# Kernel tuning notes

Hardware: AMD Instinct MI355X
Metric: run time of the kernel (lower is better)

The kernel has to match this reference:

```python
import jax, jax.numpy as jnp
import numpy as np

EPS = 1e-3  # batch_norm_epsilon


def _lstm_last(xs, W, U, b):
    """Keras-order LSTM (gates i,f,g,o); returns last hidden state [B,H]."""
    B = xs.shape[0]
    H = U.shape[0]

    def step(carry, xt):
        h, c = carry
        z = xt @ W + h @ U + b  # [B, 4H]
        i, f, g, o = jnp.split(z, 4, axis=-1)
        i = jax.nn.sigmoid(i)
        f = jax.nn.sigmoid(f)
        g = jnp.tanh(g)
        o = jax.nn.sigmoid(o)
        c = f * c + i * g
        h = o * jnp.tanh(c)
        return (h, c), None

    init = (jnp.zeros((B, H), xs.dtype), jnp.zeros((B, H), xs.dtype))
    (h, _), _ = jax.lax.scan(step, init, jnp.swapaxes(xs, 0, 1))
    return h


def setup_inputs() -> dict:
    key = jax.random.key(0)
    ks = jax.random.split(key, 10)
    B, T, C, H = 32, 512, 512, 512
    s_in = 1.0 / np.sqrt(C)
    s_rec = 1.0 / np.sqrt(H)
    return {
        "x": jax.random.normal(ks[0], (B, T, C), jnp.float32),
        # BatchNorm params (inference / moving stats)
        "gamma": jnp.ones((C,), jnp.float32),
        "beta": jnp.zeros((C,), jnp.float32),
        "moving_mean": jax.random.normal(ks[1], (C,), jnp.float32) * 0.1,
        "moving_var": jnp.abs(jax.random.normal(ks[2], (C,), jnp.float32)) * 0.1 + 1.0,
        # forward-direction LSTM
        "Wf": jax.random.normal(ks[3], (C, 4 * H), jnp.float32) * s_in,
        "Uf": jax.random.normal(ks[4], (H, 4 * H), jnp.float32) * s_rec,
        "bf": jnp.zeros((4 * H,), jnp.float32),
        # backward-direction LSTM
        "Wb": jax.random.normal(ks[5], (C, 4 * H), jnp.float32) * s_in,
        "Ub": jax.random.normal(ks[6], (H, 4 * H), jnp.float32) * s_rec,
        "bb": jnp.zeros((4 * H,), jnp.float32),
    }


def reference(x, gamma, beta, moving_mean, moving_var, Wf, Uf, bf, Wb, Ub, bb):
    # BatchNorm (inference) over last axis
    inv = jax.lax.rsqrt(moving_var + EPS)
    xn = (x - moving_mean) * inv * gamma + beta
    # Bidirectional LSTM, merge_mode='concat', return_sequences=False
    h_fwd = _lstm_last(xn, Wf, Uf, bf)
    h_bwd = _lstm_last(xn[:, ::-1, :], Wb, Ub, bb)
    return jnp.concatenate([h_fwd, h_bwd], axis=-1)  # [B, 2H]
```

## Files before the change

### kernel.cpp

```cpp
#include <hip/hip_runtime.h>
#include <stdint.h>

typedef __attribute__((ext_vector_type(8))) short short8;
typedef __attribute__((ext_vector_type(4))) float f32x4;
typedef __attribute__((ext_vector_type(2))) float f32x2;
typedef __attribute__((ext_vector_type(4))) unsigned int u32x4;
typedef __attribute__((ext_vector_type(2))) unsigned int u32x2;

#define NB 32
#define NBH 16
#define NT 512
#define NC 512
#define NH 512
#define NG 2048
#define WPG 16
#define NWG 64
#define UPW 32

__device__ __forceinline__ float bf2f(unsigned short u){
  union { unsigned int i; float f; } v; v.i = ((unsigned int)u) << 16; return v.f;
}
__device__ __forceinline__ unsigned short f2bf(float f){
  union { float f; unsigned int i; } v; v.f = f;
  unsigned int r = v.i + 0x7fffu + ((v.i >> 16) & 1u);
  return (unsigned short)(r >> 16);
}
__device__ __forceinline__ bool dt_fp32(const void* gamma){
  return ((const unsigned short*)gamma)[0] != 0x3F80;
}
__device__ __forceinline__ float ldv(const void* p, size_t i, bool f32){
  return f32 ? ((const float*)p)[i] : bf2f(((const unsigned short*)p)[i]);
}
__device__ __forceinline__ short8 frag_from_f32(const float* p){
  short8 r;
  #pragma unroll
  for (int j = 0; j < 8; ++j) r[j] = (short)f2bf(p[j]);
  return r;
}
__device__ __forceinline__ float sigm(float x){ return 1.f/(1.f + __expf(-x)); }
__device__ __forceinline__ float tanh_(float x){ return 1.f - 2.f/(1.f + __expf(2.f*x)); }

__device__ __forceinline__ unsigned int permhi(unsigned int hi, unsigned int lo){
  return __builtin_amdgcn_perm(hi, lo, 0x07060302u);
}

__device__ __forceinline__ unsigned int llc_load_u32(const unsigned int* p){
  unsigned int r;
  asm volatile("global_load_dword %0, %1, off sc0 sc1\n\ts_waitcnt vmcnt(0)"
               : "=v"(r) : "v"(p) : "memory");
  return r;
}
__device__ __forceinline__ void llc_store_u32(unsigned int* p, unsigned int v){
  asm volatile("global_store_dword %0, %1, off sc0 sc1" :: "v"(p), "v"(v) : "memory");
}
__device__ __forceinline__ void tag_load(const unsigned int* p0, u32x4 r[8]){
  asm volatile(
    "global_load_dwordx4 %0, %8, off sc0 sc1\n\t"
    "global_load_dwordx4 %1, %8, off offset:16 sc0 sc1\n\t"
    "global_load_dwordx4 %2, %8, off offset:128 sc0 sc1\n\t"
    "global_load_dwordx4 %3, %8, off offset:144 sc0 sc1\n\t"
    "global_load_dwordx4 %4, %8, off offset:256 sc0 sc1\n\t"
    "global_load_dwordx4 %5, %8, off offset:272 sc0 sc1\n\t"
    "global_load_dwordx4 %6, %8, off offset:384 sc0 sc1\n\t"
    "global_load_dwordx4 %7, %8, off offset:400 sc0 sc1\n\t"
    "s_waitcnt vmcnt(0)"
    : "=&v"(r[0]), "=&v"(r[1]), "=&v"(r[2]), "=&v"(r[3]),
      "=&v"(r[4]), "=&v"(r[5]), "=&v"(r[6]), "=&v"(r[7])
    : "v"(p0) : "memory");
}
__device__ __forceinline__ void tag_store(unsigned int* p, unsigned int lo, unsigned int hi){
  u32x2 v; v[0] = lo; v[1] = hi;
  asm volatile("global_store_dwordx2 %0, %1, off sc0 sc1" :: "v"(p), "v"(v) : "memory");
}

__global__ void k_init(const void* __restrict__ gamma,
                       const void* __restrict__ beta,
                       const void* __restrict__ mmean,
                       const void* __restrict__ mvar,
                       float* __restrict__ scale, float* __restrict__ shift,
                       unsigned int* __restrict__ hbuf, unsigned int* __restrict__ flags){
  bool f32 = dt_fp32(gamma);
  int tid = blockIdx.x * 256 + threadIdx.x;
  if (blockIdx.x == 0){
    for (int c = threadIdx.x; c < NC; c += 256){
      float s = ldv(gamma, c, f32) * rsqrtf(ldv(mvar, c, f32) + 1e-3f);
      scale[c] = s;
      shift[c] = ldv(beta, c, f32) - ldv(mmean, c, f32) * s;
    }
    if (threadIdx.x < 128) flags[threadIdx.x] = 0u;
  }
  for (int i = tid; i < 4*2*NBH*NH; i += gridDim.x * 256) hbuf[i] = 0u;
}

__global__ void k_xcast(const void* __restrict__ x, const void* __restrict__ gamma,
                        unsigned short* __restrict__ x2){
  bool f32 = dt_fp32(gamma);
  int i = blockIdx.x * 256 + threadIdx.x;
  int c8 = i & 63;
  int rest = i >> 6;
  int t = rest & (NT - 1);
  int b = rest >> 9;
  size_t src = ((size_t)b * NT + t) * NC + c8 * 8;
  size_t dst = ((size_t)t * NB + b) * NC + c8 * 8;
  unsigned int pk[4];
  if (f32){
    const float* p = (const float*)x + src;
    #pragma unroll
    for (int j = 0; j < 4; ++j)
      pk[j] = (unsigned int)f2bf(p[2*j]) | ((unsigned int)f2bf(p[2*j+1]) << 16);
  } else {
    __builtin_memcpy(pk, (const unsigned short*)x + src, 16);
  }
  __builtin_memcpy(x2 + dst, pk, 16);
}

__global__ __launch_bounds__(256, 1) void k_lstm(
    const void* __restrict__ x, const unsigned short* __restrict__ x2, int use_x2,
    const void* __restrict__ Wf, const void* __restrict__ Uf,
    const void* __restrict__ Wb, const void* __restrict__ Ub,
    const void* __restrict__ bfv, const void* __restrict__ bbv,
    const void* __restrict__ gamma,
    const float* __restrict__ scale, const float* __restrict__ shift,
    unsigned int* __restrict__ hbuf, unsigned int* __restrict__ flags,
    void* __restrict__ out){
  __shared__ float zbuf[4][NBH][132];
  __shared__ float fscr[256];
  __shared__ float fb[128];

  bool f32 = dt_fp32(gamma);
  int wg   = blockIdx.x;
  int dir  = wg & 1;
  int half = (wg >> 1) & 1;
  int wgd  = wg >> 2;
  int gidx = wg & 3;
  int ubase = wgd * UPW;
  const void* W = dir ? Wb : Wf;
  const void* U = dir ? Ub : Uf;
  const void* bvec = dir ? bbv : bfv;
  int tid  = threadIdx.x;
  int lane = tid & 63, wave = tid >> 6;
  int m = lane & 15, q = lane >> 4;

  short8 bw[4][8], bu[4][8];
  #pragma unroll
  for (int kcl = 0; kcl < 4; ++kcl){
    int kc = wave * 4 + kcl;
    #pragma unroll
    for (int nt = 0; nt < 8; ++nt){
      int col = (nt >> 1) * NH + ubase + (nt & 1) * 16 + m;
      short8 vw, vu;
      #pragma unroll
      for (int j = 0; j < 8; ++j){
        int k = kc * 32 + q * 8 + j;
        vu[j] = (short)f2bf(ldv(U, (size_t)k * NG + col, f32));
        vw[j] = (short)f2bf(scale[k] * ldv(W, (size_t)k * NG + col, f32));
      }
      bw[kcl][nt] = vw; bu[kcl][nt] = vu;
    }
  }

  {
    int cidx = tid >> 1, kh = tid & 1;
    int col = (cidx >> 5) * NH + ubase + (cidx & 31);
    float a = 0.f;
    for (int k = kh * 256; k < kh * 256 + 256; ++k)
      a += shift[k] * ldv(W, (size_t)k * NG + col, f32);
    fscr[tid] = a;
    __syncthreads();
    if (tid < 128)
      fb[tid] = fscr[2*tid] + fscr[2*tid+1]
              + ldv(bvec, (tid >> 5) * NH + ubase + (tid & 31), f32);
    __syncthreads();
  }

  int pb = tid >> 4, pu2 = (tid & 15) * 2;
  float bias_r[2][4];
  #pragma unroll
  for (int j = 0; j < 2; ++j)
    #pragma unroll
    for (int g = 0; g < 4; ++g) bias_r[j][g] = fb[g * 32 + pu2 + j];
  float cst[2] = {0.f, 0.f};

  unsigned int* gflags  = flags + gidx * 32;
  unsigned int* ownflag = gflags + wgd;
  unsigned int* hb32 = hbuf + (size_t)gidx * 2 * NBH * NH;

  short8 xf[4];
  {
    int tt0 = dir ? (NT - 1) : 0;
    int b = half * 16 + m;
    #pragma unroll
    for (int kcl = 0; kcl < 4; ++kcl){
      int kc = wave * 4 + kcl;
      if (use_x2){
        size_t xi = ((size_t)tt0 * NB + b) * NC + kc * 32 + q * 8;
        __builtin_memcpy(&xf[kcl], x2 + xi, 16);
      } else {
        size_t xi = ((size_t)b * NT + tt0) * NC + kc * 32 + q * 8;
        if (f32) xf[kcl] = frag_from_f32((const float*)x + xi);
        else     __builtin_memcpy(&xf[kcl], (const unsigned short*)x + xi, 16);
      }
    }
  }

  #pragma unroll 1
  for (int t = 0; t < NT; ++t){
    const unsigned int* hcur = hb32 + (size_t)(t & 1) * NBH * NH;
    unsigned int* hnext = hb32 + (size_t)((t + 1) & 1) * NBH * NH;

    f32x4 acc[8];
    #pragma unroll
    for (int nt = 0; nt < 8; ++nt) acc[nt] = (f32x4){0.f,0.f,0.f,0.f};

    #pragma unroll
    for (int kcl = 0; kcl < 4; ++kcl)
      #pragma unroll
      for (int nt = 0; nt < 8; ++nt)
        acc[nt] = __builtin_amdgcn_mfma_f32_16x16x32_bf16(xf[kcl], bw[kcl][nt], acc[nt], 0, 0, 0);

    if (t > 0){
      unsigned int tgt = (unsigned int)t;
      while (true){
        unsigned int v = llc_load_u32(gflags + (lane & 15));
        if (__all((int)(v >= tgt))) break;
      }
    }

    u32x4 raw[8];
    {
      unsigned int tg = (unsigned int)t;
      const unsigned int* p0 = hcur + (size_t)m * NH + wave * 128 + q * 8;
      while (true){
        tag_load(p0, raw);
        unsigned int d = 0;
        #pragma unroll
        for (int i = 0; i < 8; ++i)
          d |= (raw[i][0] ^ tg) | (raw[i][1] ^ tg) | (raw[i][2] ^ tg) | (raw[i][3] ^ tg);
        if (__all((int)((d & 0xffffu) == 0u))) break;
      }
    }

    if (t < NT - 1){
      int ttn = dir ? (NT - 2 - t) : (t + 1);
      int b = half * 16 + m;
      #pragma unroll
      for (int kcl = 0; kcl < 4; ++kcl){
        int kc = wave * 4 + kcl;
        if (use_x2){
          size_t xi = ((size_t)ttn * NB + b) * NC + kc * 32 + q * 8;
          __builtin_memcpy(&xf[kcl], x2 + xi, 16);
        } else {
          size_t xi = ((size_t)b * NT + ttn) * NC + kc * 32 + q * 8;
          if (f32) xf[kcl] = frag_from_f32((const float*)x + xi);
          else     __builtin_memcpy(&xf[kcl], (const unsigned short*)x + xi, 16);
        }
      }
    }

    #pragma unroll
    for (int kcl = 0; kcl < 4; ++kcl){
      union { short8 s; unsigned int w[4]; } u;
      u32x4 a = raw[2 * kcl];
      u32x4 b = raw[2 * kcl + 1];
      u.w[0] = permhi(a[1], a[0]);
      u.w[1] = permhi(a[3], a[2]);
      u.w[2] = permhi(b[1], b[0]);
      u.w[3] = permhi(b[3], b[2]);
      #pragma unroll
      for (int nt = 0; nt < 8; ++nt)
        acc[nt] = __builtin_amdgcn_mfma_f32_16x16x32_bf16(u.s, bu[kcl][nt], acc[nt], 0, 0, 0);
    }

    #pragma unroll
    for (int nt = 0; nt < 8; ++nt){
      int cb = (nt >> 1) * 32 + (nt & 1) * 16 + m;
      #pragma unroll
      for (int r = 0; r < 4; ++r)
        zbuf[wave][q * 4 + r][cb] = acc[nt][r];
    }
    __syncthreads();

    float z[2][4];
    #pragma unroll
    for (int g = 0; g < 4; ++g){ z[0][g] = bias_r[0][g]; z[1][g] = bias_r[1][g]; }
    #pragma unroll
    for (int w = 0; w < 4; ++w)
      #pragma unroll
      for (int g = 0; g < 4; ++g){
        f32x2 v = *(const f32x2*)&zbuf[w][pb][g * 32 + pu2];
        z[0][g] += v[0]; z[1][g] += v[1];
      }
    float hv[2];
    #pragma unroll
    for (int j = 0; j < 2; ++j){
      float iv = sigm(z[j][0]), fv = sigm(z[j][1]), gv = tanh_(z[j][2]), ov = sigm(z[j][3]);
      cst[j] = fv * cst[j] + iv * gv;
      hv[j] = ov * tanh_(cst[j]);
    }

    if (t == NT - 1){
      size_t o0 = (size_t)(half * 16 + pb) * (2 * NH) + dir * NH + ubase + pu2;
      if (f32){
        f32x2 ov2 = {hv[0], hv[1]};
        *(f32x2*)&((float*)out)[o0] = ov2;
      } else {
        unsigned int pk = (unsigned int)f2bf(hv[0]) | ((unsigned int)f2bf(hv[1]) << 16);
        *(unsigned int*)&((unsigned short*)out)[o0] = pk;
      }
      break;
    }

    {
      unsigned int tag1 = (unsigned int)(t + 1);
      unsigned int w0 = ((unsigned int)f2bf(hv[0]) << 16) | tag1;
      unsigned int w1 = ((unsigned int)f2bf(hv[1]) << 16) | tag1;
      tag_store(hnext + (size_t)pb * NH + ubase + pu2, w0, w1);
      if (tid == 0) llc_store_u32(ownflag, tag1);
    }
  }
}

extern "C" void kernel_launch(void* const* d_in, const int* in_sizes, int n_in,
                              void* d_out, int out_size, void* d_ws, size_t ws_size,
                              hipStream_t stream){
  const void* x     = d_in[0];
  const void* gamma = d_in[1];
  const void* beta  = d_in[2];
  const void* mmean = d_in[3];
  const void* mvar  = d_in[4];
  const void* Wf    = d_in[5];
  const void* Uf    = d_in[6];
  const void* bfv   = d_in[7];
  const void* Wb    = d_in[8];
  const void* Ub    = d_in[9];
  const void* bbv   = d_in[10];

  char* ws = (char*)d_ws;
  float* scale = (float*)(ws + 0);
  float* shift = (float*)(ws + 2048);
  unsigned int* hbuf  = (unsigned int*)(ws + 20480);
  unsigned int* flags = (unsigned int*)(ws + 20480 + 262144);
  size_t x2_off = 20480 + 262144 + 4096;
  unsigned short* x2 = (unsigned short*)(ws + x2_off);
  size_t x2_bytes = (size_t)NT * NB * NC * 2;
  int use_x2 = (ws_size >= x2_off + x2_bytes) ? 1 : 0;

  hipLaunchKernelGGL(k_init, dim3(64),  dim3(256), 0, stream,
                     gamma, beta, mmean, mvar, scale, shift, hbuf, flags);
  if (use_x2)
    hipLaunchKernelGGL(k_xcast, dim3((NB*NT*NC/8)/256), dim3(256), 0, stream,
                       x, gamma, x2);
  hipLaunchKernelGGL(k_lstm, dim3(NWG), dim3(256), 0, stream,
                     x, x2, use_x2, Wf, Uf, Wb, Ub, bfv, bbv, gamma, scale, shift,
                     hbuf, flags, d_out);
}
```

Baseline: 1.974 ms.

## Speculatively prefetch tagged hidden state and fold init into cast kernel

Each LSTM step now issues the tagged hidden-state loads speculatively at the start of the step, overlapping them with the input-projection MFMAs and the next x prefetch. The flag poll and reload happen only when the tags do not match. The per-step flag store is moved after a __syncthreads. The init kernel is also merged into the x cast kernel, removing one launch. This is meant to take flag-polling latency off the serial recurrence critical path, at the cost of a block barrier every step and some redundant loads when the speculation misses.

```diff
diff --git a/kernel.cpp b/kernel.cpp
--- a/kernel.cpp
+++ b/kernel.cpp
@@ -53,7 +53,7 @@
 __device__ __forceinline__ void llc_store_u32(unsigned int* p, unsigned int v){
   asm volatile("global_store_dword %0, %1, off sc0 sc1" :: "v"(p), "v"(v) : "memory");
 }
-__device__ __forceinline__ void tag_load(const unsigned int* p0, u32x4 r[8]){
+__device__ __forceinline__ void spec_issue(const unsigned int* p0, u32x4 r[8]){
   asm volatile(
     "global_load_dwordx4 %0, %8, off sc0 sc1\n\t"
     "global_load_dwordx4 %1, %8, off offset:16 sc0 sc1\n\t"
@@ -62,25 +62,35 @@
     "global_load_dwordx4 %4, %8, off offset:256 sc0 sc1\n\t"
     "global_load_dwordx4 %5, %8, off offset:272 sc0 sc1\n\t"
     "global_load_dwordx4 %6, %8, off offset:384 sc0 sc1\n\t"
-    "global_load_dwordx4 %7, %8, off offset:400 sc0 sc1\n\t"
-    "s_waitcnt vmcnt(0)"
+    "global_load_dwordx4 %7, %8, off offset:400 sc0 sc1"
     : "=&v"(r[0]), "=&v"(r[1]), "=&v"(r[2]), "=&v"(r[3]),
       "=&v"(r[4]), "=&v"(r[5]), "=&v"(r[6]), "=&v"(r[7])
     : "v"(p0) : "memory");
 }
+__device__ __forceinline__ void spec_wait4(u32x4 r[8]){
+  asm volatile("s_waitcnt vmcnt(4)"
+    : "+v"(r[0]), "+v"(r[1]), "+v"(r[2]), "+v"(r[3]),
+      "+v"(r[4]), "+v"(r[5]), "+v"(r[6]), "+v"(r[7]) :: "memory");
+}
+__device__ __forceinline__ void spec_wait0(u32x4 r[8]){
+  asm volatile("s_waitcnt vmcnt(0)"
+    : "+v"(r[0]), "+v"(r[1]), "+v"(r[2]), "+v"(r[3]),
+      "+v"(r[4]), "+v"(r[5]), "+v"(r[6]), "+v"(r[7]) :: "memory");
+}
 __device__ __forceinline__ void tag_store(unsigned int* p, unsigned int lo, unsigned int hi){
   u32x2 v; v[0] = lo; v[1] = hi;
   asm volatile("global_store_dwordx2 %0, %1, off sc0 sc1" :: "v"(p), "v"(v) : "memory");
 }
 
-__global__ void k_init(const void* __restrict__ gamma,
-                       const void* __restrict__ beta,
-                       const void* __restrict__ mmean,
-                       const void* __restrict__ mvar,
-                       float* __restrict__ scale, float* __restrict__ shift,
-                       unsigned int* __restrict__ hbuf, unsigned int* __restrict__ flags){
+__global__ void k_xcast(const void* __restrict__ x, const void* __restrict__ gamma,
+                        const void* __restrict__ beta,
+                        const void* __restrict__ mmean,
+                        const void* __restrict__ mvar,
+                        float* __restrict__ scale, float* __restrict__ shift,
+                        unsigned int* __restrict__ hbuf, unsigned int* __restrict__ flags,
+                        unsigned short* __restrict__ x2, int do_x2){
   bool f32 = dt_fp32(gamma);
-  int tid = blockIdx.x * 256 + threadIdx.x;
+  int i = blockIdx.x * 256 + threadIdx.x;
   if (blockIdx.x == 0){
     for (int c = threadIdx.x; c < NC; c += 256){
       float s = ldv(gamma, c, f32) * rsqrtf(ldv(mvar, c, f32) + 1e-3f);
@@ -89,13 +99,8 @@
     }
     if (threadIdx.x < 128) flags[threadIdx.x] = 0u;
   }
-  for (int i = tid; i < 4*2*NBH*NH; i += gridDim.x * 256) hbuf[i] = 0u;
-}
-
-__global__ void k_xcast(const void* __restrict__ x, const void* __restrict__ gamma,
-                        unsigned short* __restrict__ x2){
-  bool f32 = dt_fp32(gamma);
-  int i = blockIdx.x * 256 + threadIdx.x;
+  for (int k = i; k < 4*2*NBH*NH; k += gridDim.x * 256) hbuf[k] = 0u;
+  if (!do_x2) return;
   int c8 = i & 63;
   int rest = i >> 6;
   int t = rest & (NT - 1);
@@ -207,6 +212,10 @@
   for (int t = 0; t < NT; ++t){
     const unsigned int* hcur = hb32 + (size_t)(t & 1) * NBH * NH;
     unsigned int* hnext = hb32 + (size_t)((t + 1) & 1) * NBH * NH;
+    const unsigned int* p0 = hcur + (size_t)m * NH + wave * 128 + q * 8;
+
+    u32x4 raw[8];
+    spec_issue(p0, raw);
 
     f32x4 acc[8];
     #pragma unroll
@@ -217,28 +226,6 @@
       #pragma unroll
       for (int nt = 0; nt < 8; ++nt)
         acc[nt] = __builtin_amdgcn_mfma_f32_16x16x32_bf16(xf[kcl], bw[kcl][nt], acc[nt], 0, 0, 0);
-
-    if (t > 0){
-      unsigned int tgt = (unsigned int)t;
-      while (true){
-        unsigned int v = llc_load_u32(gflags + (lane & 15));
-        if (__all((int)(v >= tgt))) break;
-      }
-    }
-
-    u32x4 raw[8];
-    {
-      unsigned int tg = (unsigned int)t;
-      const unsigned int* p0 = hcur + (size_t)m * NH + wave * 128 + q * 8;
-      while (true){
-        tag_load(p0, raw);
-        unsigned int d = 0;
-        #pragma unroll
-        for (int i = 0; i < 8; ++i)
-          d |= (raw[i][0] ^ tg) | (raw[i][1] ^ tg) | (raw[i][2] ^ tg) | (raw[i][3] ^ tg);
-        if (__all((int)((d & 0xffffu) == 0u))) break;
-      }
-    }
 
     if (t < NT - 1){
       int ttn = dir ? (NT - 2 - t) : (t + 1);
@@ -256,6 +243,32 @@
         }
       }
     }
+    __builtin_amdgcn_sched_barrier(0);
+
+    if (t < NT - 1) spec_wait4(raw); else spec_wait0(raw);
+    __builtin_amdgcn_sched_barrier(0);
+    {
+      unsigned int tg = (unsigned int)t;
+      unsigned int d = 0;
+      #pragma unroll
+      for (int i = 0; i < 8; ++i)
+        d |= (raw[i][0] ^ tg) | (raw[i][1] ^ tg) | (raw[i][2] ^ tg) | (raw[i][3] ^ tg);
+      if (!__all((int)((d & 0xffffu) == 0u))){
+        while (true){
+          unsigned int v = llc_load_u32(gflags + (lane & 15));
+          if (__all((int)(v >= tg))) break;
+        }
+        while (true){
+          spec_issue(p0, raw);
+          spec_wait0(raw);
+          unsigned int d2 = 0;
+          #pragma unroll
+          for (int i = 0; i < 8; ++i)
+            d2 |= (raw[i][0] ^ tg) | (raw[i][1] ^ tg) | (raw[i][2] ^ tg) | (raw[i][3] ^ tg);
+          if (__all((int)((d2 & 0xffffu) == 0u))) break;
+        }
+      }
+    }
 
     #pragma unroll
     for (int kcl = 0; kcl < 4; ++kcl){
@@ -315,8 +328,9 @@
       unsigned int w0 = ((unsigned int)f2bf(hv[0]) << 16) | tag1;
       unsigned int w1 = ((unsigned int)f2bf(hv[1]) << 16) | tag1;
       tag_store(hnext + (size_t)pb * NH + ubase + pu2, w0, w1);
-      if (tid == 0) llc_store_u32(ownflag, tag1);
-    }
+    }
+    __syncthreads();
+    if (tid == 0) llc_store_u32(ownflag, (unsigned int)(t + 1));
   }
 }
 
@@ -345,11 +359,9 @@
   size_t x2_bytes = (size_t)NT * NB * NC * 2;
   int use_x2 = (ws_size >= x2_off + x2_bytes) ? 1 : 0;
 
-  hipLaunchKernelGGL(k_init, dim3(64),  dim3(256), 0, stream,
-                     gamma, beta, mmean, mvar, scale, shift, hbuf, flags);
-  if (use_x2)
-    hipLaunchKernelGGL(k_xcast, dim3((NB*NT*NC/8)/256), dim3(256), 0, stream,
-                       x, gamma, x2);
+  int xgrid = use_x2 ? (NB*NT*NC/8)/256 : 64;
+  hipLaunchKernelGGL(k_xcast, dim3(xgrid), dim3(256), 0, stream,
+                     x, gamma, beta, mmean, mvar, scale, shift, hbuf, flags, x2, use_x2);
   hipLaunchKernelGGL(k_lstm, dim3(NWG), dim3(256), 0, stream,
                      x, x2, use_x2, Wf, Uf, Wb, Ub, bfv, bbv, gamma, scale, shift,
                      hbuf, flags, d_out);
```

Result: slower. 2.369 ms (+20.0%).
